# Optimization experiments

Hardware: AMD Instinct MI355X
Metric: run time of the kernel (lower is better)

Reference implementation:

```python
import jax, jax.numpy as jnp
import numpy as np

THRESHOLD = 0.05

def binarize101(w, threshold):
    # Ternary quantization to {-1, 0, +1}: zero inside the dead-zone [-thr, thr].
    pos = (w > threshold).astype(w.dtype)
    neg = (w < -threshold).astype(w.dtype)
    return pos - neg

def setup_inputs() -> dict:
    key = jax.random.key(0)
    k1, k2, k3 = jax.random.split(key, 3)
    x = jax.random.normal(k1, (8192, 4096), dtype=jnp.float32)
    weight = jax.random.normal(k2, (4096, 4096), dtype=jnp.float32)
    bias = jax.random.normal(k3, (4096,), dtype=jnp.float32)
    return {"x": x, "weight": weight, "bias": bias}

def reference(x, weight, bias):
    wb = binarize101(weight, THRESHOLD)
    # F.linear: x @ wb.T + bias ; x: [N, in], weight: [out, in] -> [N, out]
    return jnp.einsum('ni,oi->no', x, wb) + bias
```

## Files before the change

### kernel.cpp

```cpp
#include <hip/hip_runtime.h>

typedef float floatx4 __attribute__((ext_vector_type(4)));
typedef __bf16 bf16x8 __attribute__((ext_vector_type(8)));
using u16 = unsigned short;
using u32 = unsigned int;

#define GLOBAL_AS __attribute__((address_space(1)))
#define LDS_AS    __attribute__((address_space(3)))

__global__ void cvt_x_kernel(const float* __restrict__ x, u16* __restrict__ xb, int n8) {
  int stride = gridDim.x * blockDim.x;
  for (int i = blockIdx.x * blockDim.x + threadIdx.x; i < n8; i += stride) {
    const float4* p = (const float4*)(x + (size_t)i * 8);
    float4 a = p[0], b = p[1];
    float v[8] = {a.x, a.y, a.z, a.w, b.x, b.y, b.z, b.w};
    u32 r[8];
#pragma unroll
    for (int j = 0; j < 8; ++j) {
      u32 u = __float_as_uint(v[j]);
      r[j] = (u + 0x7FFFu + ((u >> 16) & 1u)) >> 16;
    }
    uint4 o;
    o.x = r[0] | (r[1] << 16);
    o.y = r[2] | (r[3] << 16);
    o.z = r[4] | (r[5] << 16);
    o.w = r[6] | (r[7] << 16);
    *(uint4*)(xb + (size_t)i * 8) = o;
  }
}

__global__ void quant_w_kernel(const float* __restrict__ w, u16* __restrict__ wb, int n8) {
  int stride = gridDim.x * blockDim.x;
  for (int i = blockIdx.x * blockDim.x + threadIdx.x; i < n8; i += stride) {
    const float4* p = (const float4*)(w + (size_t)i * 8);
    float4 a = p[0], b = p[1];
    float v[8] = {a.x, a.y, a.z, a.w, b.x, b.y, b.z, b.w};
    u32 r[8];
#pragma unroll
    for (int j = 0; j < 8; ++j) {
      r[j] = (v[j] > 0.05f) ? 0x3F80u : ((v[j] < -0.05f) ? 0xBF80u : 0u);
    }
    uint4 o;
    o.x = r[0] | (r[1] << 16);
    o.y = r[2] | (r[3] << 16);
    o.z = r[4] | (r[5] << 16);
    o.w = r[6] | (r[7] << 16);
    *(uint4*)(wb + (size_t)i * 8) = o;
  }
}

__global__ __launch_bounds__(512, 2) void gemm_bin_m201(
    const u16* __restrict__ A, const u16* __restrict__ B,
    const float* __restrict__ bias, float* __restrict__ C,
    int M, int N, int K) {
  __shared__ u16 lds[65536];

  const int tid = threadIdx.x;
  const int w = tid >> 6, l = tid & 63;
  const int wr = w >> 2, wc = w & 3;
  const int r = l & 15;

  const int nbn = N >> 8;
  int wg = blockIdx.x;
  const int nwg = gridDim.x;
  if ((nwg & 7) == 0) wg = (wg & 7) * (nwg >> 3) + (wg >> 3);
  const int bm = wg / nbn, bn = wg % nbn;

  const int T = K >> 6;

  const int srow = ((tid >> 7) << 4) + (tid & 15);
  const int skk = (((tid >> 6) & 1) << 5) + (((tid >> 4) & 3) << 3);
  const size_t aLo0 = (size_t)(bm * 256 + srow) * K + skk;
  const int brow = ((tid >> 8) << 6) + (((tid >> 7) & 1) << 4) + (tid & 15);
  const size_t bLo0 = (size_t)(bn * 256 + brow) * K + skk;
  const size_t cs = (size_t)128 * K;

  floatx4 acc[8][4] = {};
  bf16x8 af[8], bflo[4], bfhi[4];

#define GLOAD(gptr, u16off)                                                    \
  __builtin_amdgcn_global_load_lds((const GLOBAL_AS void*)(gptr),              \
                                   (LDS_AS void*)(lds + (u16off)), 16, 0, 0)
#define BARRIER __builtin_amdgcn_s_barrier()
#define LGKM0  do { asm volatile("s_waitcnt lgkmcnt(0)" ::: "memory");         \
                    __builtin_amdgcn_sched_barrier(0); } while (0)

  GLOAD(A + aLo0,               0 + tid * 8);
  GLOAD(A + aLo0 + cs,       8192 + tid * 8);
  GLOAD(B + bLo0,           16384 + tid * 8);
  GLOAD(B + bLo0 + cs,      20480 + tid * 8);
  GLOAD(B + bLo0 + (size_t)32 * K,      24576 + tid * 8);
  GLOAD(B + bLo0 + (size_t)32 * K + cs, 28672 + tid * 8);
  GLOAD(A + aLo0 + (size_t)64 * K,       4096 + tid * 8);
  GLOAD(A + aLo0 + (size_t)64 * K + cs, 12288 + tid * 8);
  asm volatile("s_waitcnt vmcnt(4)" ::: "memory");
  BARRIER;

  for (int t = 0; t < T; ++t) {
    const int bufc = (t & 1) << 15;
    const int bufn = bufc ^ 32768;
    const bool doSt = (t + 1 < T);
    const size_t kadv = (size_t)(t + 1) << 6;

    const u16* afp = lds + bufc + wr * 8192 + l * 8;
    const u16* bfp = lds + bufc + 16384 + wc * 2048 + l * 8;

#pragma unroll
    for (int i = 0; i < 8; ++i) af[i] = *(const bf16x8*)(afp + i * 512);
#pragma unroll
    for (int i = 0; i < 4; ++i) bflo[i] = *(const bf16x8*)(bfp + i * 512);
    if (doSt) {
      GLOAD(A + aLo0 + kadv,      bufn + 0 + tid * 8);
      GLOAD(A + aLo0 + cs + kadv, bufn + 8192 + tid * 8);
    }
    asm volatile("s_waitcnt lgkmcnt(8)" ::: "memory");
    BARRIER;
    LGKM0;
    __builtin_amdgcn_s_setprio(1);
#pragma unroll
    for (int j = 0; j < 2; ++j)
#pragma unroll
      for (int mg = 0; mg < 4; ++mg)
#pragma unroll
        for (int ng = 0; ng < 2; ++ng)
          acc[mg][ng] = __builtin_amdgcn_mfma_f32_16x16x32_bf16(
              af[mg * 2 + j], bflo[ng * 2 + j], acc[mg][ng], 0, 0, 0);
    __builtin_amdgcn_s_setprio(0);
    if (doSt) asm volatile("s_waitcnt vmcnt(4)" ::: "memory");
    else      asm volatile("s_waitcnt vmcnt(2)" ::: "memory");
    BARRIER;

#pragma unroll
    for (int i = 0; i < 4; ++i) bfhi[i] = *(const bf16x8*)(bfp + 8192 + i * 512);
    if (doSt) {
      GLOAD(B + bLo0 + kadv,      bufn + 16384 + tid * 8);
      GLOAD(B + bLo0 + cs + kadv, bufn + 20480 + tid * 8);
    }
    BARRIER;
    LGKM0;
    __builtin_amdgcn_s_setprio(1);
#pragma unroll
    for (int j = 0; j < 2; ++j)
#pragma unroll
      for (int mg = 0; mg < 4; ++mg)
#pragma unroll
        for (int ng = 0; ng < 2; ++ng)
          acc[mg][2 + ng] = __builtin_amdgcn_mfma_f32_16x16x32_bf16(
              af[mg * 2 + j], bfhi[ng * 2 + j], acc[mg][2 + ng], 0, 0, 0);
    __builtin_amdgcn_s_setprio(0);
    if (doSt) asm volatile("s_waitcnt vmcnt(4)" ::: "memory");
    else      asm volatile("s_waitcnt vmcnt(0)" ::: "memory");
    BARRIER;

#pragma unroll
    for (int i = 0; i < 8; ++i) af[i] = *(const bf16x8*)(afp + 4096 + i * 512);
    if (doSt) {
      GLOAD(B + bLo0 + (size_t)32 * K + kadv,      bufn + 24576 + tid * 8);
      GLOAD(B + bLo0 + (size_t)32 * K + cs + kadv, bufn + 28672 + tid * 8);
    }
    asm volatile("s_waitcnt lgkmcnt(4)" ::: "memory");
    BARRIER;
    LGKM0;
    __builtin_amdgcn_s_setprio(1);
#pragma unroll
    for (int j = 0; j < 2; ++j)
#pragma unroll
      for (int mg = 0; mg < 4; ++mg)
#pragma unroll
        for (int ng = 0; ng < 2; ++ng)
          acc[4 + mg][ng] = __builtin_amdgcn_mfma_f32_16x16x32_bf16(
              af[mg * 2 + j], bflo[ng * 2 + j], acc[4 + mg][ng], 0, 0, 0);
    __builtin_amdgcn_s_setprio(0);
    if (doSt) asm volatile("s_waitcnt vmcnt(4)" ::: "memory");
    BARRIER;

    if (doSt) {
      GLOAD(A + aLo0 + (size_t)64 * K + kadv,      bufn + 4096 + tid * 8);
      GLOAD(A + aLo0 + (size_t)64 * K + cs + kadv, bufn + 12288 + tid * 8);
    }
    BARRIER;
    __builtin_amdgcn_s_setprio(1);
#pragma unroll
    for (int j = 0; j < 2; ++j)
#pragma unroll
      for (int mg = 0; mg < 4; ++mg)
#pragma unroll
        for (int ng = 0; ng < 2; ++ng)
          acc[4 + mg][2 + ng] = __builtin_amdgcn_mfma_f32_16x16x32_bf16(
              af[mg * 2 + j], bfhi[ng * 2 + j], acc[4 + mg][2 + ng], 0, 0, 0);
    __builtin_amdgcn_s_setprio(0);
    if (doSt) asm volatile("s_waitcnt vmcnt(4)" ::: "memory");
    BARRIER;
  }
#undef GLOAD
#undef BARRIER
#undef LGKM0

  const int g = l >> 4;
  const int colb = bn * 256 + wc * 64;
  float bv[4];
#pragma unroll
  for (int n = 0; n < 4; ++n) bv[n] = bias[colb + n * 16 + r];
  const int rowb0 = bm * 256 + wr * 128;
#pragma unroll
  for (int m = 0; m < 8; ++m) {
    const int rowb = rowb0 + m * 16 + g * 4;
#pragma unroll
    for (int n = 0; n < 4; ++n) {
      const int col = colb + n * 16 + r;
      float* cp = C + (size_t)rowb * N + col;
#pragma unroll
      for (int q = 0; q < 4; ++q) cp[(size_t)q * N] = acc[m][n][q] + bv[n];
    }
  }
}

__global__ void gemm_naive_kernel(const float* __restrict__ x, const float* __restrict__ wgt,
                                  const float* __restrict__ bias, float* __restrict__ out,
                                  int M, int N, int K) {
  long long idx = (long long)blockIdx.x * blockDim.x + threadIdx.x;
  if (idx >= (long long)M * N) return;
  int o = (int)(idx % N);
  int m = (int)(idx / N);
  const float* xr = x + (size_t)m * K;
  const float* wr = wgt + (size_t)o * K;
  float s = 0.f;
  for (int i = 0; i < K; ++i) {
    float wv = wr[i];
    float t = (wv > 0.05f) ? 1.f : ((wv < -0.05f) ? -1.f : 0.f);
    s = fmaf(xr[i], t, s);
  }
  out[idx] = s + bias[o];
}

extern "C" void kernel_launch(void* const* d_in, const int* in_sizes, int n_in,
                              void* d_out, int out_size, void* d_ws, size_t ws_size,
                              hipStream_t stream) {
  const float* x    = (const float*)d_in[0];
  const float* wgt  = (const float*)d_in[1];
  const float* bias = (const float*)d_in[2];
  float* out = (float*)d_out;

  const int N = in_sizes[2];
  const int K = in_sizes[1] / N;
  const int M = in_sizes[0] / K;

  const size_t need = ((size_t)M * K + (size_t)N * K) * sizeof(u16);
  if (ws_size >= need && (M % 256 == 0) && (N % 256 == 0) && (K % 64 == 0) && K >= 128) {
    u16* xb = (u16*)d_ws;
    u16* wb = xb + (size_t)M * K;
    const int nx8 = (M * K) / 8;
    const int nw8 = (N * K) / 8;
    cvt_x_kernel<<<2048, 256, 0, stream>>>(x, xb, nx8);
    quant_w_kernel<<<2048, 256, 0, stream>>>(wgt, wb, nw8);
    const int grid = (M / 256) * (N / 256);
    gemm_bin_m201<<<grid, 512, 0, stream>>>(xb, wb, bias, out, M, N, K);
  } else {
    const long long total = (long long)M * N;
    gemm_naive_kernel<<<(unsigned)((total + 255) / 256), 256, 0, stream>>>(x, wgt, bias, out, M, N, K);
  }
}
```

Baseline: 307.4 us.

## Pre-permute bf16 operands into tile-contiguous layout for linear GEMM loads

The conversion and quantization kernels now write x and the ternary weights in a blocked layout that matches the GEMM's LDS tile order, so each 256-row by 64-k tile is contiguous. The GEMM then loads each chunk with fully contiguous 16-byte-per-lane addresses instead of strided row accesses, which is meant to improve global-load coalescing and reduce address arithmetic and TLB/cache-line spread. The prepass kernels now do scattered writes and an integer divide per element, which may slow them.

```diff
diff --git a/kernel.cpp b/kernel.cpp
--- a/kernel.cpp
+++ b/kernel.cpp
@@ -8,10 +8,13 @@
 #define GLOBAL_AS __attribute__((address_space(1)))
 #define LDS_AS    __attribute__((address_space(3)))
 
-__global__ void cvt_x_kernel(const float* __restrict__ x, u16* __restrict__ xb, int n8) {
+__global__ void cvt_x_perm(const float* __restrict__ x, u16* __restrict__ xb,
+                           int K, int Kd8, int n8) {
   int stride = gridDim.x * blockDim.x;
   for (int i = blockIdx.x * blockDim.x + threadIdx.x; i < n8; i += stride) {
-    const float4* p = (const float4*)(x + (size_t)i * 8);
+    const int row = i / Kd8;
+    const int k = (i - row * Kd8) * 8;
+    const float4* p = (const float4*)(x + (size_t)row * K + k);
     float4 a = p[0], b = p[1];
     float v[8] = {a.x, a.y, a.z, a.w, b.x, b.y, b.z, b.w};
     u32 r[8];
@@ -25,14 +28,22 @@
     o.y = r[2] | (r[3] << 16);
     o.z = r[4] | (r[5] << 16);
     o.w = r[6] | (r[7] << 16);
-    *(uint4*)(xb + (size_t)i * 8) = o;
-  }
-}
-
-__global__ void quant_w_kernel(const float* __restrict__ w, u16* __restrict__ wb, int n8) {
+    const int pn = row >> 8, rl = row & 255;
+    const int g = rl >> 6, rr = rl & 63;
+    const int t = k >> 6, kl = k & 63;
+    const int tid = ((rr >> 4) << 7) | (((kl >> 5) & 1) << 6) | (((kl >> 3) & 3) << 4) | (rr & 15);
+    u16* dst = xb + (size_t)pn * ((size_t)K << 8) + (size_t)t * 16384 + g * 4096 + tid * 8;
+    *(uint4*)dst = o;
+  }
+}
+
+__global__ void quant_w_perm(const float* __restrict__ w, u16* __restrict__ wb,
+                             int K, int Kd8, int n8) {
   int stride = gridDim.x * blockDim.x;
   for (int i = blockIdx.x * blockDim.x + threadIdx.x; i < n8; i += stride) {
-    const float4* p = (const float4*)(w + (size_t)i * 8);
+    const int n = i / Kd8;
+    const int k = (i - n * Kd8) * 8;
+    const float4* p = (const float4*)(w + (size_t)n * K + k);
     float4 a = p[0], b = p[1];
     float v[8] = {a.x, a.y, a.z, a.w, b.x, b.y, b.z, b.w};
     u32 r[8];
@@ -45,12 +56,18 @@
     o.y = r[2] | (r[3] << 16);
     o.z = r[4] | (r[5] << 16);
     o.w = r[6] | (r[7] << 16);
-    *(uint4*)(wb + (size_t)i * 8) = o;
-  }
-}
-
-__global__ __launch_bounds__(512, 2) void gemm_bin_m201(
-    const u16* __restrict__ A, const u16* __restrict__ B,
+    const int pn = n >> 8, rl = n & 255;
+    const int q = ((rl >> 7) & 1) + (((rl >> 5) & 1) << 1);
+    const int t = k >> 6, kl = k & 63;
+    const int tid = (((rl >> 6) & 1) << 8) | (((rl >> 4) & 1) << 7) |
+                    (((kl >> 5) & 1) << 6) | (((kl >> 3) & 3) << 4) | (rl & 15);
+    u16* dst = wb + (size_t)pn * ((size_t)K << 8) + (size_t)t * 16384 + q * 4096 + tid * 8;
+    *(uint4*)dst = o;
+  }
+}
+
+__global__ __launch_bounds__(512, 2) void gemm_bin_lin(
+    const u16* __restrict__ Ap, const u16* __restrict__ Bp,
     const float* __restrict__ bias, float* __restrict__ C,
     int M, int N, int K) {
   __shared__ u16 lds[65536];
@@ -68,12 +85,11 @@
 
   const int T = K >> 6;
 
-  const int srow = ((tid >> 7) << 4) + (tid & 15);
-  const int skk = (((tid >> 6) & 1) << 5) + (((tid >> 4) & 3) << 3);
-  const size_t aLo0 = (size_t)(bm * 256 + srow) * K + skk;
-  const int brow = ((tid >> 8) << 6) + (((tid >> 7) & 1) << 4) + (tid & 15);
-  const size_t bLo0 = (size_t)(bn * 256 + brow) * K + skk;
-  const size_t cs = (size_t)128 * K;
+  const u16* const Abase = Ap + (size_t)bm * ((size_t)K << 8) + tid * 8;
+  const u16* const Bbase = Bp + (size_t)bn * ((size_t)K << 8) + tid * 8;
+
+  const u16* const afp0 = lds + wr * 8192 + l * 8;
+  const u16* const bfp0 = lds + 16384 + wc * 2048 + l * 8;
 
   floatx4 acc[8][4] = {};
   bf16x8 af[8], bflo[4], bfhi[4];
@@ -85,14 +101,14 @@
 #define LGKM0  do { asm volatile("s_waitcnt lgkmcnt(0)" ::: "memory");         \
                     __builtin_amdgcn_sched_barrier(0); } while (0)
 
-  GLOAD(A + aLo0,               0 + tid * 8);
-  GLOAD(A + aLo0 + cs,       8192 + tid * 8);
-  GLOAD(B + bLo0,           16384 + tid * 8);
-  GLOAD(B + bLo0 + cs,      20480 + tid * 8);
-  GLOAD(B + bLo0 + (size_t)32 * K,      24576 + tid * 8);
-  GLOAD(B + bLo0 + (size_t)32 * K + cs, 28672 + tid * 8);
-  GLOAD(A + aLo0 + (size_t)64 * K,       4096 + tid * 8);
-  GLOAD(A + aLo0 + (size_t)64 * K + cs, 12288 + tid * 8);
+  GLOAD(Abase + 0 * 4096,      0 + tid * 8);
+  GLOAD(Abase + 2 * 4096,   8192 + tid * 8);
+  GLOAD(Bbase + 0 * 4096,  16384 + tid * 8);
+  GLOAD(Bbase + 1 * 4096,  20480 + tid * 8);
+  GLOAD(Bbase + 2 * 4096,  24576 + tid * 8);
+  GLOAD(Bbase + 3 * 4096,  28672 + tid * 8);
+  GLOAD(Abase + 1 * 4096,   4096 + tid * 8);
+  GLOAD(Abase + 3 * 4096,  12288 + tid * 8);
   asm volatile("s_waitcnt vmcnt(4)" ::: "memory");
   BARRIER;
 
@@ -100,18 +116,18 @@
     const int bufc = (t & 1) << 15;
     const int bufn = bufc ^ 32768;
     const bool doSt = (t + 1 < T);
-    const size_t kadv = (size_t)(t + 1) << 6;
-
-    const u16* afp = lds + bufc + wr * 8192 + l * 8;
-    const u16* bfp = lds + bufc + 16384 + wc * 2048 + l * 8;
+    const size_t tn = (size_t)(t + 1) * 16384;
+
+    const u16* afp = afp0 + bufc;
+    const u16* bfp = bfp0 + bufc;
 
 #pragma unroll
     for (int i = 0; i < 8; ++i) af[i] = *(const bf16x8*)(afp + i * 512);
 #pragma unroll
     for (int i = 0; i < 4; ++i) bflo[i] = *(const bf16x8*)(bfp + i * 512);
     if (doSt) {
-      GLOAD(A + aLo0 + kadv,      bufn + 0 + tid * 8);
-      GLOAD(A + aLo0 + cs + kadv, bufn + 8192 + tid * 8);
+      GLOAD(Abase + tn + 0 * 4096, bufn + 0 + tid * 8);
+      GLOAD(Abase + tn + 2 * 4096, bufn + 8192 + tid * 8);
     }
     asm volatile("s_waitcnt lgkmcnt(8)" ::: "memory");
     BARRIER;
@@ -133,8 +149,8 @@
 #pragma unroll
     for (int i = 0; i < 4; ++i) bfhi[i] = *(const bf16x8*)(bfp + 8192 + i * 512);
     if (doSt) {
-      GLOAD(B + bLo0 + kadv,      bufn + 16384 + tid * 8);
-      GLOAD(B + bLo0 + cs + kadv, bufn + 20480 + tid * 8);
+      GLOAD(Bbase + tn + 0 * 4096, bufn + 16384 + tid * 8);
+      GLOAD(Bbase + tn + 1 * 4096, bufn + 20480 + tid * 8);
     }
     BARRIER;
     LGKM0;
@@ -155,8 +171,8 @@
 #pragma unroll
     for (int i = 0; i < 8; ++i) af[i] = *(const bf16x8*)(afp + 4096 + i * 512);
     if (doSt) {
-      GLOAD(B + bLo0 + (size_t)32 * K + kadv,      bufn + 24576 + tid * 8);
-      GLOAD(B + bLo0 + (size_t)32 * K + cs + kadv, bufn + 28672 + tid * 8);
+      GLOAD(Bbase + tn + 2 * 4096, bufn + 24576 + tid * 8);
+      GLOAD(Bbase + tn + 3 * 4096, bufn + 28672 + tid * 8);
     }
     asm volatile("s_waitcnt lgkmcnt(4)" ::: "memory");
     BARRIER;
@@ -175,8 +191,8 @@
     BARRIER;
 
     if (doSt) {
-      GLOAD(A + aLo0 + (size_t)64 * K + kadv,      bufn + 4096 + tid * 8);
-      GLOAD(A + aLo0 + (size_t)64 * K + cs + kadv, bufn + 12288 + tid * 8);
+      GLOAD(Abase + tn + 1 * 4096, bufn + 4096 + tid * 8);
+      GLOAD(Abase + tn + 3 * 4096, bufn + 12288 + tid * 8);
     }
     BARRIER;
     __builtin_amdgcn_s_setprio(1);
@@ -251,10 +267,10 @@
     u16* wb = xb + (size_t)M * K;
     const int nx8 = (M * K) / 8;
     const int nw8 = (N * K) / 8;
-    cvt_x_kernel<<<2048, 256, 0, stream>>>(x, xb, nx8);
-    quant_w_kernel<<<2048, 256, 0, stream>>>(wgt, wb, nw8);
+    cvt_x_perm<<<2048, 256, 0, stream>>>(x, xb, K, K / 8, nx8);
+    quant_w_perm<<<2048, 256, 0, stream>>>(wgt, wb, K, K / 8, nw8);
     const int grid = (M / 256) * (N / 256);
-    gemm_bin_m201<<<grid, 512, 0, stream>>>(xb, wb, bias, out, M, N, K);
+    gemm_bin_lin<<<grid, 512, 0, stream>>>(xb, wb, bias, out, M, N, K);
   } else {
     const long long total = (long long)M * N;
     gemm_naive_kernel<<<(unsigned)((total + 255) / 256), 256, 0, stream>>>(x, wgt, bias, out, M, N, K);
```

New measurement: 357.0 us. +16.1%, slower.
